# Kernel optimization log

Measured on AMD Instinct MI355X. Metric: run time of the kernel, lower is better.

The kernel has to match this reference:

```python
import jax, jax.numpy as jnp
import numpy as np

HIDDEN = 2048
HEADS = 16
HEAD_DIM = HIDDEN // HEADS  # 128


def setup_inputs() -> dict:
    key = jax.random.key(0)
    ks = jax.random.split(key, 9)
    B, S = 2, 2048
    std = 0.02
    return {
        "hidden_states": jax.random.normal(ks[0], (B, S, HIDDEN), jnp.float32),
        "wq": jax.random.normal(ks[1], (HIDDEN, HIDDEN), jnp.float32) * std,
        "bq": jnp.zeros((HIDDEN,), jnp.float32),
        "wk": jax.random.normal(ks[2], (HIDDEN, HIDDEN), jnp.float32) * std,
        "bk": jnp.zeros((HIDDEN,), jnp.float32),
        "wv": jax.random.normal(ks[3], (HIDDEN, HIDDEN), jnp.float32) * std,
        "bv": jnp.zeros((HIDDEN,), jnp.float32),
        "wo": jax.random.normal(ks[4], (HIDDEN, HIDDEN), jnp.float32) * std,
        "bo": jnp.zeros((HIDDEN,), jnp.float32),
    }


def _split_heads(x):
    B, S, _ = x.shape
    return x.reshape(B, S, HEADS, HEAD_DIM).transpose(0, 2, 1, 3)


def reference(hidden_states, wq, bq, wk, bk, wv, bv, wo, bo):
    B, S, _ = hidden_states.shape
    q = _split_heads(hidden_states @ wq + bq)  # [B,H,S,D]
    k = _split_heads(hidden_states @ wk + bk)
    v = _split_heads(hidden_states @ wv + bv)
    # Original blocks q/k/v and applies softmax over axes (m, j) jointly,
    # which normalizes over the full kv axis -> identical to standard softmax attention.
    scores = jnp.einsum('bhqd,bhkd->bhqk', q, k) / jnp.sqrt(jnp.float32(HEAD_DIM))
    attn = jax.nn.softmax(scores, axis=-1)
    out = jnp.einsum('bhqk,bhkd->bhqd', attn, v)
    out = out.transpose(0, 2, 1, 3).reshape(B, S, HIDDEN)
    return out @ wo + bo
```

## Files before the change

kernel.cpp:

```cpp
#include <hip/hip_runtime.h>

typedef unsigned short u16;
typedef unsigned int u32;
typedef __bf16 bf16x8 __attribute__((ext_vector_type(8)));
typedef float f32x4 __attribute__((ext_vector_type(4)));
typedef float f32x16 __attribute__((ext_vector_type(16)));
typedef u16 u16x4v __attribute__((ext_vector_type(4)));
typedef u16 u16x8v __attribute__((ext_vector_type(8)));
typedef u32 u32x4v __attribute__((ext_vector_type(4)));

#define MFMA16(a, b, c) __builtin_amdgcn_mfma_f32_16x16x32_bf16((a), (b), (c), 0, 0, 0)
#define MFMA32(a, b, c) __builtin_amdgcn_mfma_f32_32x32x16_bf16((a), (b), (c), 0, 0, 0)

__device__ __forceinline__ u16 bfc(float f) {
  __bf16 h = (__bf16)f;
  return __builtin_bit_cast(u16, h);
}

__device__ __forceinline__ u32 cvtpk(float a, float b) {
  u32 r;
  asm("v_cvt_pk_bf16_f32 %0, %1, %2" : "=v"(r) : "v"(a), "v"(b));
  return r;
}

__device__ __forceinline__ void pswap(u32& a, u32& b) {
  asm volatile("v_permlane32_swap_b32 %0, %1" : "+v"(a), "+v"(b));
}

__device__ __forceinline__ bf16x8 ld_bf8(const u16* p) {
  u16x8v t = *(const u16x8v*)p;
  return __builtin_bit_cast(bf16x8, t);
}

__device__ __forceinline__ void gl_lds16(const u16* g, u16* l) {
  __builtin_amdgcn_global_load_lds(
      (const __attribute__((address_space(1))) u32*)(const void*)g,
      (__attribute__((address_space(3))) u32*)(void*)l, 16, 0, 0);
}

__global__ __launch_bounds__(256) void cast_bf16(const float* __restrict__ in,
                                                 u16* __restrict__ out, int n4) {
  int idx = blockIdx.x * 256 + threadIdx.x;
  int stride = gridDim.x * 256;
  for (int i = idx; i < n4; i += stride) {
    float4 v = ((const float4*)in)[i];
    u16x4v o = {bfc(v.x), bfc(v.y), bfc(v.z), bfc(v.w)};
    *(u16x4v*)(out + (size_t)i * 4) = o;
  }
}

__global__ __launch_bounds__(256) void cast_transpose4(const float* __restrict__ w0,
                                                       const float* __restrict__ w1,
                                                       const float* __restrict__ w2,
                                                       const float* __restrict__ w3,
                                                       u16* __restrict__ dst) {
  const int R = 2048, C = 2048;
  const float* W = blockIdx.z == 0 ? w0 : blockIdx.z == 1 ? w1 : blockIdx.z == 2 ? w2 : w3;
  u16* WT = dst + (size_t)blockIdx.z * R * C;
  __shared__ float t[32][33];
  int bx = blockIdx.x * 32, by = blockIdx.y * 32;
  int tx = threadIdx.x, ty = threadIdx.y;
#pragma unroll
  for (int i = 0; i < 4; i++)
    t[ty + i * 8][tx] = W[(size_t)(by + ty + i * 8) * C + bx + tx];
  __syncthreads();
#pragma unroll
  for (int i = 0; i < 4; i++)
    WT[(size_t)(bx + ty + i * 8) * R + by + tx] = bfc(t[tx][ty + i * 8]);
}

__global__ __launch_bounds__(256) void transpose_bf16s(const u16* __restrict__ V,
                                                       u16* __restrict__ VT, int R, int C,
                                                       int src_stride) {
  __shared__ u16 t[32][33];
  int bx = blockIdx.x * 32, by = blockIdx.y * 32;
  int tx = threadIdx.x, ty = threadIdx.y;
#pragma unroll
  for (int i = 0; i < 4; i++)
    t[ty + i * 8][tx] = V[(size_t)(by + ty + i * 8) * src_stride + bx + tx];
  __syncthreads();
#pragma unroll
  for (int i = 0; i < 4; i++)
    VT[(size_t)(bx + ty + i * 8) * R + by + tx] = t[tx][ty + i * 8];
}

#define GSTAGE(buf_, k0_)                                                          \
  {                                                                                \
    _Pragma("unroll") for (int i = 0; i < 4; i++) {                                \
      gl_lds16(aw + (size_t)(i * 8 + srow) * K + (k0_) + scol,                     \
               &As[buf_][wid * 32 + i * 8][0]);                                    \
      gl_lds16(bw + (size_t)(i * 8 + srow) * K + (k0_) + scol,                     \
               &Bs[buf_][wid * 32 + i * 8][0]);                                    \
    }                                                                              \
  }

template <bool OUT_F32>
__global__ __launch_bounds__(256) void gemm_bt(const u16* __restrict__ A,
                                               const u16* __restrict__ BT,
                                               const float* __restrict__ bias,
                                               void* __restrict__ Cout,
                                               int M, int N, int K, float alpha) {
  __shared__ u16 As[2][128][64];
  __shared__ u16 Bs[2][128][64];
  const int tid = threadIdx.x;
  const int lane = tid & 63, wid = tid >> 6;
  const int wm = wid >> 1, wn = wid & 1;
  const int bm0 = blockIdx.y * 128, bn0 = blockIdx.x * 128;
  const int lr = lane & 15, lg = lane >> 4;

  const int srow = lane >> 3;
  const int scol = (lane & 7) * 8;
  const u16* aw = A + (size_t)(bm0 + wid * 32) * K;
  const u16* bw = BT + (size_t)(bn0 + wid * 32) * K;

  f32x4 acc[4][4] = {};

  const int NT = K >> 6;
  GSTAGE(0, 0);
  __syncthreads();

  for (int t = 0; t < NT; t++) {
    const int buf = t & 1;
    if (t + 1 < NT) GSTAGE(buf ^ 1, (t + 1) * 64);
#pragma unroll
    for (int kk = 0; kk < 2; kk++) {
      bf16x8 af[4], bfr[4];
#pragma unroll
      for (int i = 0; i < 4; i++)
        af[i] = ld_bf8(&As[buf][wm * 64 + i * 16 + lr][kk * 32 + lg * 8]);
#pragma unroll
      for (int j = 0; j < 4; j++)
        bfr[j] = ld_bf8(&Bs[buf][wn * 64 + j * 16 + lr][kk * 32 + lg * 8]);
#pragma unroll
      for (int i = 0; i < 4; i++)
#pragma unroll
        for (int j = 0; j < 4; j++)
          acc[i][j] = MFMA16(af[i], bfr[j], acc[i][j]);
    }
    __syncthreads();
  }

#pragma unroll
  for (int i = 0; i < 4; i++) {
#pragma unroll
    for (int j = 0; j < 4; j++) {
      int col = bn0 + wn * 64 + j * 16 + lr;
      float bv = bias[col];
#pragma unroll
      for (int r = 0; r < 4; r++) {
        int row = bm0 + wm * 64 + i * 16 + lg * 4 + r;
        float v = alpha * (acc[i][j][r] + bv);
        if (OUT_F32)
          ((float*)Cout)[(size_t)row * N + col] = v;
        else
          ((u16*)Cout)[(size_t)row * N + col] = bfc(v);
      }
    }
  }
}


#define STAGE(buf_, kv0_)                                                        \
  {                                                                              \
    _Pragma("unroll") for (int ii = 0; ii < 2; ii++) {                           \
      int i_ = w * 2 + ii;                                                       \
      int kr_ = i_ * 4 + (lane >> 4);                                            \
      int kc_ = (lane & 15) ^ (kr_ & 15);                                        \
      gl_lds16(K + (size_t)(b * 2048 + (kv0_) + kr_) * 2048 + h * 128 + kc_ * 8, \
               &Ks[buf_][i_ * 4][0]);                                            \
      int vr_ = i_ * 8 + (lane >> 3);                                            \
      int vc_ = (lane & 7) ^ (vr_ & 7);                                          \
      gl_lds16(VT + (size_t)(h * 128 + vr_) * MT + b * 2048 + (kv0_) + vc_ * 8,  \
               &Vs[buf_][i_ * 8][0]);                                            \
    }                                                                            \
  }

#define PFRAGS(p_, pfA, pfB)                                                    \
  {                                                                             \
    u32 w_[8];                                                                  \
    _Pragma("unroll") for (int T = 0; T < 4; T++) {                             \
      w_[2 * T] = cvtpk(p_[4 * T], p_[4 * T + 1]);                              \
      w_[2 * T + 1] = cvtpk(p_[4 * T + 2], p_[4 * T + 3]);                      \
    }                                                                           \
    pswap(w_[0], w_[2]);                                                        \
    pswap(w_[1], w_[3]);                                                        \
    pswap(w_[4], w_[6]);                                                        \
    pswap(w_[5], w_[7]);                                                        \
    u32x4v fA = {w_[0], w_[1], w_[2], w_[3]};                                   \
    pfA = __builtin_bit_cast(bf16x8, fA);                                       \
    u32x4v fB = {w_[4], w_[5], w_[6], w_[7]};                                   \
    pfB = __builtin_bit_cast(bf16x8, fB);                                       \
  }

#define CTILE(buf_)                                                             \
  {                                                                             \
    f32x16 s0 = {}, s1 = {};                                                    \
    _Pragma("unroll") for (int c = 0; c < 8; c++) {                             \
      bf16x8 kf = ld_bf8(&Ks[buf_][ql][((2 * c + hi) ^ (ql & 15)) * 8]);        \
      s0 = MFMA32(kf, qf[c], s0);                                               \
    }                                                                           \
    _Pragma("unroll") for (int c = 0; c < 8; c++) {                             \
      bf16x8 kf = ld_bf8(&Ks[buf_][32 + ql][((2 * c + hi) ^ (ql & 15)) * 8]);   \
      s1 = MFMA32(kf, qf[c], s1);                                               \
    }                                                                           \
    float p0[16], p1[16];                                                       \
    _Pragma("unroll") for (int r = 0; r < 16; r++) {                            \
      p0[r] = __builtin_exp2f(s0[r]);                                           \
      p1[r] = __builtin_exp2f(s1[r]);                                           \
    }                                                                           \
    bf16x8 pf[4];                                                               \
    PFRAGS(p0, pf[0], pf[1]);                                                   \
    PFRAGS(p1, pf[2], pf[3]);                                                   \
    _Pragma("unroll") for (int c = 0; c < 4; c++)                               \
        ol = MFMA32(onesf, pf[c], ol);                                          \
    _Pragma("unroll") for (int dk = 0; dk < 4; dk++) {                          \
      _Pragma("unroll") for (int c = 0; c < 4; c++) {                           \
        bf16x8 vf = ld_bf8(&Vs[buf_][dk * 32 + ql][((2 * c + hi) ^ (ql & 7)) * 8]); \
        o[dk] = MFMA32(vf, pf[c], o[dk]);                                       \
      }                                                                         \
    }                                                                           \
  }

__global__ __launch_bounds__(512, 2) void attn_lds(const u16* __restrict__ Q,
                                                   const u16* __restrict__ K,
                                                   const u16* __restrict__ VT,
                                                   u16* __restrict__ Ctx) {
  const int MT = 4096;
  __shared__ u16 Ks[2][64][128];
  __shared__ u16 Vs[2][128][64];

  const int tid = threadIdx.x;
  const int lane = tid & 63, w = tid >> 6;
  const int ql = lane & 31, hi = lane >> 5;

  const int bid = blockIdx.x;
  const int nid = (bid & 7) * 32 + (bid >> 3);
  const int bh = nid >> 3, qt = nid & 7;
  const int b = bh >> 4, h = bh & 15;
  const int q0 = qt * 256 + w * 32;

  bf16x8 qf[8];
  {
    const u16* qp = Q + (size_t)(b * 2048 + q0 + ql) * 2048 + h * 128 + hi * 8;
#pragma unroll
    for (int c = 0; c < 8; c++) qf[c] = ld_bf8(qp + c * 16);
  }

  bf16x8 onesf;
  {
    u32x4v ov = {0x3F803F80u, 0x3F803F80u, 0x3F803F80u, 0x3F803F80u};
    onesf = __builtin_bit_cast(bf16x8, ov);
  }

  f32x16 o[4] = {};
  f32x16 ol = {};

  STAGE(0, 0);
  __syncthreads();

  for (int t = 0; t < 32; t++) {
    const int buf = t & 1;
    if (t < 31) STAGE(buf ^ 1, (t + 1) * 64);
    CTILE(buf);
    __syncthreads();
  }

  float rn = 1.f / ol[0];
  u16* cp = Ctx + (size_t)(b * 2048 + q0 + ql) * 2048 + h * 128;
#pragma unroll
  for (int dblk = 0; dblk < 4; dblk++) {
#pragma unroll
    for (int g = 0; g < 4; g++) {
      u16x4v ov = {bfc(o[dblk][4 * g] * rn), bfc(o[dblk][4 * g + 1] * rn),
                   bfc(o[dblk][4 * g + 2] * rn), bfc(o[dblk][4 * g + 3] * rn)};
      *(u16x4v*)(cp + dblk * 32 + g * 8 + hi * 4) = ov;
    }
  }
}

extern "C" void kernel_launch(void* const* d_in, const int* in_sizes, int n_in,
                              void* d_out, int out_size, void* d_ws, size_t ws_size,
                              hipStream_t stream) {
  const float* X  = (const float*)d_in[0];
  const float* wq = (const float*)d_in[1];
  const float* bq = (const float*)d_in[2];
  const float* wk = (const float*)d_in[3];
  const float* bk = (const float*)d_in[4];
  const float* wv = (const float*)d_in[5];
  const float* bv = (const float*)d_in[6];
  const float* wo = (const float*)d_in[7];
  const float* bo = (const float*)d_in[8];
  float* out = (float*)d_out;

  const size_t M = 4096, H = 2048;
  u16* ws  = (u16*)d_ws;
  u16* Xb  = ws;
  u16* WqT = Xb  + M * H;
  u16* WkT = WqT + H * H;
  u16* WvT = WkT + H * H;
  u16* WoT = WvT + H * H;
  u16* Qb  = WoT + H * H;
  u16* Kb  = Qb  + M * H;
  u16* Vb  = Kb  + M * H;
  u16* VbT = Vb  + M * H;
  u16* Cx  = VbT + M * H;

  dim3 tb(32, 8);

  cast_bf16<<<2048, 256, 0, stream>>>(X, Xb, (int)(M * H / 4));
  cast_transpose4<<<dim3(64, 64, 4), tb, 0, stream>>>(wq, wk, wv, wo, WqT);

  const float alpha_q = 0.12751744f;
  gemm_bt<false><<<dim3(16, 32), 256, 0, stream>>>(Xb, WqT, bq, (void*)Qb, 4096, 2048, 2048, alpha_q);
  gemm_bt<false><<<dim3(16, 32), 256, 0, stream>>>(Xb, WkT, bk, (void*)Kb, 4096, 2048, 2048, 1.0f);
  gemm_bt<false><<<dim3(16, 32), 256, 0, stream>>>(Xb, WvT, bv, (void*)Vb, 4096, 2048, 2048, 1.0f);

  transpose_bf16s<<<dim3(64, 128), tb, 0, stream>>>(Vb, VbT, 4096, 2048, 2048);

  attn_lds<<<256, 512, 0, stream>>>(Qb, Kb, VbT, Cx);

  gemm_bt<true><<<dim3(16, 32), 256, 0, stream>>>(Cx, WoT, bo, (void*)out, 4096, 2048, 2048, 1.0f);
}
```

Before: 307.4 us.

## Fuse V transpose into V projection epilogue and remap GEMM block order

The V projection GEMM now writes its output already transposed, with 4 bf16 values per vector store, so the separate bf16 transpose kernel and its intermediate buffer are gone. All GEMMs switch to a 1D grid with a block-index remap that spreads consecutive blocks across the XCDs, changing which tiles each XCD's L2 holds. This removes one kernel launch plus a full read and write of V. The transposed stores stride by M per column, which may coalesce worse than the row-major stores.

```diff
diff --git a/kernel.cpp b/kernel.cpp
--- a/kernel.cpp
+++ b/kernel.cpp
@@ -69,21 +69,6 @@
     WT[(size_t)(bx + ty + i * 8) * R + by + tx] = bfc(t[tx][ty + i * 8]);
 }
 
-__global__ __launch_bounds__(256) void transpose_bf16s(const u16* __restrict__ V,
-                                                       u16* __restrict__ VT, int R, int C,
-                                                       int src_stride) {
-  __shared__ u16 t[32][33];
-  int bx = blockIdx.x * 32, by = blockIdx.y * 32;
-  int tx = threadIdx.x, ty = threadIdx.y;
-#pragma unroll
-  for (int i = 0; i < 4; i++)
-    t[ty + i * 8][tx] = V[(size_t)(by + ty + i * 8) * src_stride + bx + tx];
-  __syncthreads();
-#pragma unroll
-  for (int i = 0; i < 4; i++)
-    VT[(size_t)(bx + ty + i * 8) * R + by + tx] = t[tx][ty + i * 8];
-}
-
 #define GSTAGE(buf_, k0_)                                                          \
   {                                                                                \
     _Pragma("unroll") for (int i = 0; i < 4; i++) {                                \
@@ -94,7 +79,7 @@
     }                                                                              \
   }
 
-template <bool OUT_F32>
+template <int OMODE>
 __global__ __launch_bounds__(256) void gemm_bt(const u16* __restrict__ A,
                                                const u16* __restrict__ BT,
                                                const float* __restrict__ bias,
@@ -105,8 +90,12 @@
   const int tid = threadIdx.x;
   const int lane = tid & 63, wid = tid >> 6;
   const int wm = wid >> 1, wn = wid & 1;
-  const int bm0 = blockIdx.y * 128, bn0 = blockIdx.x * 128;
   const int lr = lane & 15, lg = lane >> 4;
+
+  const int bid = blockIdx.x;
+  const int nid = (bid & 7) * 64 + (bid >> 3);
+  const int bm0 = (nid & 31) * 128;
+  const int bn0 = (nid >> 5) * 128;
 
   const int srow = lane >> 3;
   const int scol = (lane & 7) * 8;
@@ -146,14 +135,20 @@
     for (int j = 0; j < 4; j++) {
       int col = bn0 + wn * 64 + j * 16 + lr;
       float bv = bias[col];
-#pragma unroll
-      for (int r = 0; r < 4; r++) {
-        int row = bm0 + wm * 64 + i * 16 + lg * 4 + r;
-        float v = alpha * (acc[i][j][r] + bv);
-        if (OUT_F32)
-          ((float*)Cout)[(size_t)row * N + col] = v;
-        else
-          ((u16*)Cout)[(size_t)row * N + col] = bfc(v);
+      int row0 = bm0 + wm * 64 + i * 16 + lg * 4;
+      if (OMODE == 2) {
+        u16x4v ov = {bfc(alpha * (acc[i][j][0] + bv)), bfc(alpha * (acc[i][j][1] + bv)),
+                     bfc(alpha * (acc[i][j][2] + bv)), bfc(alpha * (acc[i][j][3] + bv))};
+        *(u16x4v*)((u16*)Cout + (size_t)col * M + row0) = ov;
+      } else {
+#pragma unroll
+        for (int r = 0; r < 4; r++) {
+          float v = alpha * (acc[i][j][r] + bv);
+          if (OMODE == 1)
+            ((float*)Cout)[(size_t)(row0 + r) * N + col] = v;
+          else
+            ((u16*)Cout)[(size_t)(row0 + r) * N + col] = bfc(v);
+        }
       }
     }
   }
@@ -301,9 +296,8 @@
   u16* WoT = WvT + H * H;
   u16* Qb  = WoT + H * H;
   u16* Kb  = Qb  + M * H;
-  u16* Vb  = Kb  + M * H;
-  u16* VbT = Vb  + M * H;
-  u16* Cx  = VbT + M * H;
+  u16* VbT = Kb  + M * H;
+  u16* Cx  = VbT + H * M;
 
   dim3 tb(32, 8);
 
@@ -311,13 +305,11 @@
   cast_transpose4<<<dim3(64, 64, 4), tb, 0, stream>>>(wq, wk, wv, wo, WqT);
 
   const float alpha_q = 0.12751744f;
-  gemm_bt<false><<<dim3(16, 32), 256, 0, stream>>>(Xb, WqT, bq, (void*)Qb, 4096, 2048, 2048, alpha_q);
-  gemm_bt<false><<<dim3(16, 32), 256, 0, stream>>>(Xb, WkT, bk, (void*)Kb, 4096, 2048, 2048, 1.0f);
-  gemm_bt<false><<<dim3(16, 32), 256, 0, stream>>>(Xb, WvT, bv, (void*)Vb, 4096, 2048, 2048, 1.0f);
-
-  transpose_bf16s<<<dim3(64, 128), tb, 0, stream>>>(Vb, VbT, 4096, 2048, 2048);
+  gemm_bt<0><<<512, 256, 0, stream>>>(Xb, WqT, bq, (void*)Qb, 4096, 2048, 2048, alpha_q);
+  gemm_bt<0><<<512, 256, 0, stream>>>(Xb, WkT, bk, (void*)Kb, 4096, 2048, 2048, 1.0f);
+  gemm_bt<2><<<512, 256, 0, stream>>>(Xb, WvT, bv, (void*)VbT, 4096, 2048, 2048, 1.0f);
 
   attn_lds<<<256, 512, 0, stream>>>(Qb, Kb, VbT, Cx);
 
-  gemm_bt<true><<<dim3(16, 32), 256, 0, stream>>>(Cx, WoT, bo, (void*)out, 4096, 2048, 2048, 1.0f);
-}
+  gemm_bt<1><<<512, 256, 0, stream>>>(Cx, WoT, bo, (void*)out, 4096, 2048, 2048, 1.0f);
+}
```

After: 326.2 us. 1.06x slower.

## Software-pipeline attention with 4-stage LDS ring and QK/PV overlap

Applied to the files above, without the earlier changes.

Replaces the double-buffered K/V LDS loop with a four-buffer ring that keeps three tiles of global-to-LDS loads in flight, synchronised by manual vmcnt waits and raw barriers. The QK^T MFMAs for the next tile are issued before the exp/PV stage of the current tile, so matrix work and softmax/VALU work can interleave. LDS usage doubles and occupancy drops to one 512-thread block per CU, which may cost latency hiding. The hand-counted vmcnt values must match the number of loads each STAGE issues, or the pipeline will read stale data.

```diff
diff --git a/kernel.cpp b/kernel.cpp
--- a/kernel.cpp
+++ b/kernel.cpp
@@ -37,6 +37,10 @@
       (const __attribute__((address_space(1))) u32*)(const void*)g,
       (__attribute__((address_space(3))) u32*)(void*)l, 16, 0, 0);
 }
+
+#define VMCNT_(n) asm volatile("s_waitcnt vmcnt(" #n ")" ::: "memory")
+#define VMCNT(n) VMCNT_(n)
+#define BARR() asm volatile("s_barrier" ::: "memory")
 
 __global__ __launch_bounds__(256) void cast_bf16(const float* __restrict__ in,
                                                  u16* __restrict__ out, int n4) {
@@ -192,21 +196,26 @@
     pfB = __builtin_bit_cast(bf16x8, fB);                                       \
   }
 
-#define CTILE(buf_)                                                             \
+#define QKT(bq_, S0p, S1p)                                                      \
   {                                                                             \
-    f32x16 s0 = {}, s1 = {};                                                    \
+    S0p = (f32x16){};                                                           \
+    S1p = (f32x16){};                                                           \
     _Pragma("unroll") for (int c = 0; c < 8; c++) {                             \
-      bf16x8 kf = ld_bf8(&Ks[buf_][ql][((2 * c + hi) ^ (ql & 15)) * 8]);        \
-      s0 = MFMA32(kf, qf[c], s0);                                               \
+      bf16x8 kf = ld_bf8(&Ks[bq_][ql][((2 * c + hi) ^ (ql & 15)) * 8]);         \
+      S0p = MFMA32(kf, qf[c], S0p);                                             \
     }                                                                           \
     _Pragma("unroll") for (int c = 0; c < 8; c++) {                             \
-      bf16x8 kf = ld_bf8(&Ks[buf_][32 + ql][((2 * c + hi) ^ (ql & 15)) * 8]);   \
-      s1 = MFMA32(kf, qf[c], s1);                                               \
-    }                                                                           \
+      bf16x8 kf = ld_bf8(&Ks[bq_][32 + ql][((2 * c + hi) ^ (ql & 15)) * 8]);    \
+      S1p = MFMA32(kf, qf[c], S1p);                                             \
+    }                                                                           \
+  }
+
+#define SMPV(bv_, S0c, S1c)                                                     \
+  {                                                                             \
     float p0[16], p1[16];                                                       \
     _Pragma("unroll") for (int r = 0; r < 16; r++) {                            \
-      p0[r] = __builtin_exp2f(s0[r]);                                           \
-      p1[r] = __builtin_exp2f(s1[r]);                                           \
+      p0[r] = __builtin_exp2f(S0c[r]);                                          \
+      p1[r] = __builtin_exp2f(S1c[r]);                                          \
     }                                                                           \
     bf16x8 pf[4];                                                               \
     PFRAGS(p0, pf[0], pf[1]);                                                   \
@@ -215,19 +224,19 @@
         ol = MFMA32(onesf, pf[c], ol);                                          \
     _Pragma("unroll") for (int dk = 0; dk < 4; dk++) {                          \
       _Pragma("unroll") for (int c = 0; c < 4; c++) {                           \
-        bf16x8 vf = ld_bf8(&Vs[buf_][dk * 32 + ql][((2 * c + hi) ^ (ql & 7)) * 8]); \
+        bf16x8 vf = ld_bf8(&Vs[bv_][dk * 32 + ql][((2 * c + hi) ^ (ql & 7)) * 8]); \
         o[dk] = MFMA32(vf, pf[c], o[dk]);                                       \
       }                                                                         \
     }                                                                           \
   }
 
-__global__ __launch_bounds__(512, 2) void attn_lds(const u16* __restrict__ Q,
+__global__ __launch_bounds__(512, 1) void attn_lds(const u16* __restrict__ Q,
                                                    const u16* __restrict__ K,
                                                    const u16* __restrict__ VT,
                                                    u16* __restrict__ Ctx) {
   const int MT = 4096;
-  __shared__ u16 Ks[2][64][128];
-  __shared__ u16 Vs[2][128][64];
+  __shared__ u16 Ks[4][64][128];
+  __shared__ u16 Vs[4][128][64];
 
   const int tid = threadIdx.x;
   const int lane = tid & 63, w = tid >> 6;
@@ -254,16 +263,58 @@
 
   f32x16 o[4] = {};
   f32x16 ol = {};
+  f32x16 SA0, SA1, SB0, SB1;
 
   STAGE(0, 0);
-  __syncthreads();
-
-  for (int t = 0; t < 32; t++) {
-    const int buf = t & 1;
-    if (t < 31) STAGE(buf ^ 1, (t + 1) * 64);
-    CTILE(buf);
-    __syncthreads();
-  }
+  STAGE(1, 64);
+  STAGE(2, 128);
+  VMCNT(4);
+  BARR();
+  QKT(0, SA0, SA1);
+
+  for (int u = 0; u < 7; u++) {
+    const int kb = u * 4;
+    STAGE(3, (kb + 3) * 64);
+    QKT(1, SB0, SB1);
+    SMPV(0, SA0, SA1);
+    VMCNT(4);
+    BARR();
+
+    STAGE(0, (kb + 4) * 64);
+    QKT(2, SA0, SA1);
+    SMPV(1, SB0, SB1);
+    VMCNT(4);
+    BARR();
+
+    STAGE(1, (kb + 5) * 64);
+    QKT(3, SB0, SB1);
+    SMPV(2, SA0, SA1);
+    VMCNT(4);
+    BARR();
+
+    STAGE(2, (kb + 6) * 64);
+    QKT(0, SA0, SA1);
+    SMPV(3, SB0, SB1);
+    VMCNT(4);
+    BARR();
+  }
+
+  STAGE(3, 31 * 64);
+  QKT(1, SB0, SB1);
+  SMPV(0, SA0, SA1);
+  VMCNT(4);
+  BARR();
+
+  QKT(2, SA0, SA1);
+  SMPV(1, SB0, SB1);
+  VMCNT(0);
+  BARR();
+
+  QKT(3, SB0, SB1);
+  SMPV(2, SA0, SA1);
+  BARR();
+
+  SMPV(3, SB0, SB1);
 
   float rn = 1.f / ol[0];
   u16* cp = Ctx + (size_t)(b * 2048 + q0 + ql) * 2048 + h * 128;
```

Measured after the change: 311.4 us. About the same (+1.3%).

## Split attention KV range across two warp groups per block and merge via LDS

Applied to the files above, without the earlier changes.

Doubles the attention block to 1024 threads, with two halves each processing half of the KV sequence (1024 keys) for the same 256 query rows. Each half has its own double-buffered K/V LDS tiles. Partial outputs and row sums are combined through shared memory at the end. This is meant to raise wave count per CU and shorten each block's serial KV loop, since only 256 blocks were launched. In exchange it uses about 129 KB of LDS per block, which limits occupancy, and adds a merge step. It relies on the unnormalized exp2 trick (no running max), so the partial sums add directly.

```diff
diff --git a/kernel.cpp b/kernel.cpp
--- a/kernel.cpp
+++ b/kernel.cpp
@@ -160,18 +160,19 @@
 }
 
 
-#define STAGE(buf_, kv0_)                                                        \
+#define STAGE(buf_, t_)                                                          \
   {                                                                              \
+    const int kv0_ = khv + (t_) * 64;                                            \
     _Pragma("unroll") for (int ii = 0; ii < 2; ii++) {                           \
-      int i_ = w * 2 + ii;                                                       \
+      int i_ = wq * 2 + ii;                                                      \
       int kr_ = i_ * 4 + (lane >> 4);                                            \
       int kc_ = (lane & 15) ^ (kr_ & 15);                                        \
-      gl_lds16(K + (size_t)(b * 2048 + (kv0_) + kr_) * 2048 + h * 128 + kc_ * 8, \
-               &Ks[buf_][i_ * 4][0]);                                            \
+      gl_lds16(K + (size_t)(b * 2048 + kv0_ + kr_) * 2048 + h * 128 + kc_ * 8,   \
+               &Ksh[buf_][i_ * 4][0]);                                           \
       int vr_ = i_ * 8 + (lane >> 3);                                            \
       int vc_ = (lane & 7) ^ (vr_ & 7);                                          \
-      gl_lds16(VT + (size_t)(h * 128 + vr_) * MT + b * 2048 + (kv0_) + vc_ * 8,  \
-               &Vs[buf_][i_ * 8][0]);                                            \
+      gl_lds16(VT + (size_t)(h * 128 + vr_) * MT + b * 2048 + kv0_ + vc_ * 8,    \
+               &Vsh[buf_][i_ * 8][0]);                                           \
     }                                                                            \
   }
 
@@ -196,11 +197,11 @@
   {                                                                             \
     f32x16 s0 = {}, s1 = {};                                                    \
     _Pragma("unroll") for (int c = 0; c < 8; c++) {                             \
-      bf16x8 kf = ld_bf8(&Ks[buf_][ql][((2 * c + hi) ^ (ql & 15)) * 8]);        \
+      bf16x8 kf = ld_bf8(&Ksh[buf_][ql][((2 * c + hi) ^ (ql & 15)) * 8]);       \
       s0 = MFMA32(kf, qf[c], s0);                                               \
     }                                                                           \
     _Pragma("unroll") for (int c = 0; c < 8; c++) {                             \
-      bf16x8 kf = ld_bf8(&Ks[buf_][32 + ql][((2 * c + hi) ^ (ql & 15)) * 8]);   \
+      bf16x8 kf = ld_bf8(&Ksh[buf_][32 + ql][((2 * c + hi) ^ (ql & 15)) * 8]);  \
       s1 = MFMA32(kf, qf[c], s1);                                               \
     }                                                                           \
     float p0[16], p1[16];                                                       \
@@ -215,29 +216,35 @@
         ol = MFMA32(onesf, pf[c], ol);                                          \
     _Pragma("unroll") for (int dk = 0; dk < 4; dk++) {                          \
       _Pragma("unroll") for (int c = 0; c < 4; c++) {                           \
-        bf16x8 vf = ld_bf8(&Vs[buf_][dk * 32 + ql][((2 * c + hi) ^ (ql & 7)) * 8]); \
+        bf16x8 vf = ld_bf8(&Vsh[buf_][dk * 32 + ql][((2 * c + hi) ^ (ql & 7)) * 8]); \
         o[dk] = MFMA32(vf, pf[c], o[dk]);                                       \
       }                                                                         \
     }                                                                           \
   }
 
-__global__ __launch_bounds__(512, 2) void attn_lds(const u16* __restrict__ Q,
-                                                   const u16* __restrict__ K,
-                                                   const u16* __restrict__ VT,
-                                                   u16* __restrict__ Ctx) {
+__global__ __launch_bounds__(1024, 4) void attn_lds(const u16* __restrict__ Q,
+                                                    const u16* __restrict__ K,
+                                                    const u16* __restrict__ VT,
+                                                    u16* __restrict__ Ctx) {
   const int MT = 4096;
-  __shared__ u16 Ks[2][64][128];
-  __shared__ u16 Vs[2][128][64];
-
+  __shared__ __align__(16) unsigned char smem[132096];
   const int tid = threadIdx.x;
   const int lane = tid & 63, w = tid >> 6;
+  const int hb = w >> 3, wq = w & 7;
   const int ql = lane & 31, hi = lane >> 5;
+  const int khv = hb * 1024;
+
+  u16 (*Ksh)[64][128] = (u16(*)[64][128])(smem + (size_t)hb * 32768);
+  u16 (*Vsh)[128][64] = (u16(*)[128][64])(smem + 65536 + (size_t)hb * 32768);
+  float* cbuf = (float*)smem;
+  float* lbuf = (float*)(smem + 131072);
 
   const int bid = blockIdx.x;
   const int nid = (bid & 7) * 32 + (bid >> 3);
   const int bh = nid >> 3, qt = nid & 7;
   const int b = bh >> 4, h = bh & 15;
-  const int q0 = qt * 256 + w * 32;
+  const int q0 = qt * 256 + wq * 32;
+  const int row = wq * 32 + ql;
 
   bf16x8 qf[8];
   {
@@ -258,22 +265,39 @@
   STAGE(0, 0);
   __syncthreads();
 
-  for (int t = 0; t < 32; t++) {
+  for (int t = 0; t < 16; t++) {
     const int buf = t & 1;
-    if (t < 31) STAGE(buf ^ 1, (t + 1) * 64);
+    if (t < 15) STAGE(buf ^ 1, t + 1);
     CTILE(buf);
     __syncthreads();
   }
 
-  float rn = 1.f / ol[0];
-  u16* cp = Ctx + (size_t)(b * 2048 + q0 + ql) * 2048 + h * 128;
-#pragma unroll
-  for (int dblk = 0; dblk < 4; dblk++) {
-#pragma unroll
-    for (int g = 0; g < 4; g++) {
-      u16x4v ov = {bfc(o[dblk][4 * g] * rn), bfc(o[dblk][4 * g + 1] * rn),
-                   bfc(o[dblk][4 * g + 2] * rn), bfc(o[dblk][4 * g + 3] * rn)};
-      *(u16x4v*)(cp + dblk * 32 + g * 8 + hi * 4) = ov;
+  __syncthreads();
+  if (hb == 0) {
+#pragma unroll
+    for (int dblk = 0; dblk < 4; dblk++)
+#pragma unroll
+      for (int g = 0; g < 4; g++)
+#pragma unroll
+        for (int j = 0; j < 4; j++)
+          cbuf[(size_t)row * 128 + dblk * 32 + g * 8 + hi * 4 + j] = o[dblk][4 * g + j];
+    if (hi == 0) lbuf[row] = ol[0];
+  }
+  __syncthreads();
+  if (hb == 1) {
+    float rn = 1.f / (lbuf[row] + ol[0]);
+    u16* cp = Ctx + (size_t)(b * 2048 + q0 + ql) * 2048 + h * 128;
+#pragma unroll
+    for (int dblk = 0; dblk < 4; dblk++) {
+#pragma unroll
+      for (int g = 0; g < 4; g++) {
+        const float* cb = &cbuf[(size_t)row * 128 + dblk * 32 + g * 8 + hi * 4];
+        u16x4v ov = {bfc((cb[0] + o[dblk][4 * g]) * rn),
+                     bfc((cb[1] + o[dblk][4 * g + 1]) * rn),
+                     bfc((cb[2] + o[dblk][4 * g + 2]) * rn),
+                     bfc((cb[3] + o[dblk][4 * g + 3]) * rn)};
+        *(u16x4v*)(cp + dblk * 32 + g * 8 + hi * 4) = ov;
+      }
     }
   }
 }
@@ -317,7 +341,7 @@
 
   transpose_bf16s<<<dim3(64, 128), tb, 0, stream>>>(Vb, VbT, 4096, 2048, 2048);
 
-  attn_lds<<<256, 512, 0, stream>>>(Qb, Kb, VbT, Cx);
+  attn_lds<<<256, 1024, 0, stream>>>(Qb, Kb, VbT, Cx);
 
   gemm_bt<true><<<dim3(16, 32), 256, 0, stream>>>(Cx, WoT, bo, (void*)out, 4096, 2048, 2048, 1.0f);
 }
```

Measured after the change: 575.6 us. 87.2% more time.
